# Kernel optimization log

Hardware: AMD Instinct MI355X
Metric: run time of the kernel (lower is better)

## Reference

```python
import jax, jax.numpy as jnp
import numpy as np

N = 8192
H = 256
E = N * 32
ALPHA = 0.2  # LeakyReLU negative slope from init kwarg alpha


def setup_inputs() -> dict:
    key = jax.random.key(0)
    ks = jax.random.split(key, 8)
    s = 1.0 / np.sqrt(H)
    return {
        "features": jax.random.normal(ks[0], (N, H), jnp.float32),
        "edge_index": jax.random.randint(ks[1], (2, E), 0, N, jnp.int64),
        "W_att": jax.random.normal(ks[2], (H, H), jnp.float32) * s,
        "a_src": jax.random.normal(ks[3], (H,), jnp.float32) * s,
        "a_dst": jax.random.normal(ks[4], (H,), jnp.float32) * s,
        "gcn_w": jax.random.normal(ks[5], (H, H), jnp.float32) * s,
        "gcn_b": jnp.zeros((H,), jnp.float32),
        "out_w": jax.random.normal(ks[6], (H, 2), jnp.float32) * s,
        "out_b": jnp.zeros((2,), jnp.float32),
    }


def reference(features, edge_index, W_att, a_src, a_dst, gcn_w, gcn_b, out_w, out_b):
    n = features.shape[0]
    # --- SingleNodeAttentionLayer (GAT-style dense self-attention, concat=True) ---
    Wh = features @ W_att                       # [N, H]
    e = jax.nn.leaky_relu(
        (Wh @ a_src)[:, None] + (Wh @ a_dst)[None, :], negative_slope=ALPHA
    )                                            # [N, N]
    attn = jax.nn.softmax(e, axis=-1)
    h1 = jax.nn.elu(attn @ Wh)                   # [N, H]
    # --- GCNConv: symmetric-normalized aggregation with self-loops ---
    loops = jnp.arange(n, dtype=edge_index.dtype)
    row = jnp.concatenate([edge_index[0], loops])  # destination
    col = jnp.concatenate([edge_index[1], loops])  # source
    deg = jax.ops.segment_sum(jnp.ones_like(row, dtype=h1.dtype), row, num_segments=n)
    dinv = jax.lax.rsqrt(jnp.maximum(deg, 1e-12))
    norm = dinv[row] * dinv[col]                 # [E+N]
    x = h1 @ gcn_w                               # [N, H]
    agg = jax.ops.segment_sum(x[col] * norm[:, None], row, num_segments=n) + gcn_b
    # --- head: linear -> mean over nodes -> softmax ---
    res = agg @ out_w + out_b                    # [N, 2]
    res = jnp.mean(res, axis=0, keepdims=True)   # [1, 2]
    return jax.nn.softmax(res, axis=-1)
```

## Files before the change

kernel.cpp:

```cpp
#include <hip/hip_runtime.h>
#include <hip/hip_bf16.h>

#define NN 8192
#define HH 256
#define EE (NN*32)
#define ALPHAC 0.2f
#define CHUNK 16
#define NCHUNK (NN/CHUNK)
#define CSPAD 1024

typedef __bf16 bf16x8 __attribute__((ext_vector_type(8)));
typedef float  f32x4  __attribute__((ext_vector_type(4)));

#define OFF_WH     0
#define OFF_S      (OFF_WH + NN*HH)
#define OFF_D      (OFF_S + NN)
#define OFF_SORTD  (OFF_D + NN)
#define OFF_PERM   (OFF_SORTD + NN)
#define OFF_EA     (OFF_PERM + NN)
#define OFF_E1     (OFF_EA + NN)
#define OFF_SAREL  (OFF_E1 + NN)
#define OFF_SBREL  (OFF_SAREL + NN)
#define OFF_ABPART (OFF_SBREL + NN)
#define OFF_CPAB   (OFF_ABPART + 2*NN*HH)
#define OFF_CSA    (OFF_CPAB + 2*(NCHUNK+1)*HH)
#define OFF_CSB    (OFF_CSA + CSPAD)
#define OFF_DEG    (OFF_CSB + CSPAD)
#define OFF_V      (OFF_DEG + NN)
#define OFF_DINV   (OFF_V + HH)
#define OFF_WNODE  (OFF_DINV + NN)
#define OFF_KEYS   (OFF_WNODE + NN)
#define OFF_FB16   (OFF_KEYS + 2*NN)
#define OFF_WT16   (OFF_FB16 + NN*HH/2)

__global__ __launch_bounds__(256) void k_prep(const float* __restrict__ features,
                                              const float* __restrict__ W_att,
                                              float* ws) {
    int bid = blockIdx.x, tid = threadIdx.x;
    if (bid < 1024) {
        int base = (bid*256 + tid)*8;
        float4 a = *(const float4*)(features + base);
        float4 b = *(const float4*)(features + base + 4);
        bf16x8 v;
        v[0]=(__bf16)a.x; v[1]=(__bf16)a.y; v[2]=(__bf16)a.z; v[3]=(__bf16)a.w;
        v[4]=(__bf16)b.x; v[5]=(__bf16)b.y; v[6]=(__bf16)b.z; v[7]=(__bf16)b.w;
        *(bf16x8*)((__bf16*)(ws + OFF_FB16) + base) = v;
    } else if (bid < 1056) {
        int idx0 = ((bid-1024)*256 + tid)*8;
        __bf16* WT = (__bf16*)(ws + OFF_WT16);
        #pragma unroll
        for (int q = 0; q < 8; ++q) {
            int idx = idx0 + q;
            int n = idx >> 8, k = idx & 255;
            WT[idx] = (__bf16)W_att[(size_t)k*HH + n];
        }
    } else {
        int z0 = ((bid-1056)*256 + tid)*8;
        #pragma unroll
        for (int q = 0; q < 8; ++q) {
            int i = z0 + q;
            if (i < NN + HH) ws[OFF_DEG + i] = 0.f;
        }
    }
}

__global__ __launch_bounds__(256) void k_gemm_deg(const int* __restrict__ ei, float* ws) {
    int bid = blockIdx.x, tid = threadIdx.x;
    if (bid < 512) {
        int mt = bid >> 2, nt = bid & 3;
        int wave = tid >> 6, lane = tid & 63;
        int ml = lane & 15, quad = lane >> 4;
        int row0 = mt*64 + wave*16;
        int n0 = nt*64;
        const __bf16* FB = (const __bf16*)(ws + OFF_FB16);
        const __bf16* WT = (const __bf16*)(ws + OFF_WT16);
        const __bf16* Ap = FB + (size_t)(row0 + ml)*HH + quad*8;
        const __bf16* B0 = WT + (size_t)(n0 +  0 + ml)*HH + quad*8;
        const __bf16* B1 = WT + (size_t)(n0 + 16 + ml)*HH + quad*8;
        const __bf16* B2 = WT + (size_t)(n0 + 32 + ml)*HH + quad*8;
        const __bf16* B3 = WT + (size_t)(n0 + 48 + ml)*HH + quad*8;
        f32x4 ac0 = {0.f,0.f,0.f,0.f}, ac1 = ac0, ac2 = ac0, ac3 = ac0;
        #pragma unroll
        for (int k0 = 0; k0 < HH; k0 += 32) {
            bf16x8 af = *(const bf16x8*)(Ap + k0);
            ac0 = __builtin_amdgcn_mfma_f32_16x16x32_bf16(af, *(const bf16x8*)(B0 + k0), ac0, 0, 0, 0);
            ac1 = __builtin_amdgcn_mfma_f32_16x16x32_bf16(af, *(const bf16x8*)(B1 + k0), ac1, 0, 0, 0);
            ac2 = __builtin_amdgcn_mfma_f32_16x16x32_bf16(af, *(const bf16x8*)(B2 + k0), ac2, 0, 0, 0);
            ac3 = __builtin_amdgcn_mfma_f32_16x16x32_bf16(af, *(const bf16x8*)(B3 + k0), ac3, 0, 0, 0);
        }
        float* Whp = ws + OFF_WH;
        #pragma unroll
        for (int r = 0; r < 4; ++r) {
            size_t grow = (size_t)(row0 + quad*4 + r)*HH + n0 + ml;
            Whp[grow +  0] = ac0[r];
            Whp[grow + 16] = ac1[r];
            Whp[grow + 32] = ac2[r];
            Whp[grow + 48] = ac3[r];
        }
    } else {
        int e = (bid - 512)*256 + tid;
        atomicAdd(ws + OFF_DEG + ei[e], 1.0f);
    }
}

__global__ __launch_bounds__(256) void k_sd_dinv2(const float* __restrict__ a_src,
                                                  const float* __restrict__ a_dst,
                                                  float* ws) {
    int bid = blockIdx.x, tid = threadIdx.x;
    if (bid < 2048) {
        int wave = tid >> 6, lane = tid & 63;
        int row = bid*4 + wave;
        const float* Wh = ws + OFF_WH;
        float4 wh = *(const float4*)(Wh + (size_t)row*HH + lane*4);
        float4 as = *(const float4*)(a_src + lane*4);
        float4 ad = *(const float4*)(a_dst + lane*4);
        float ss = wh.x*as.x + wh.y*as.y + wh.z*as.z + wh.w*as.w;
        float dd = wh.x*ad.x + wh.y*ad.y + wh.z*ad.z + wh.w*ad.w;
        #pragma unroll
        for (int off = 32; off; off >>= 1) {
            ss += __shfl_xor(ss, off);
            dd += __shfl_xor(dd, off);
        }
        if (lane == 0) {
            ws[OFF_S+row] = ss; ws[OFF_D+row] = dd;
            unsigned u = __float_as_uint(dd);
            unsigned mono = u ^ ((u & 0x80000000u) ? 0xFFFFFFFFu : 0x80000000u);
            ((unsigned long long*)(ws + OFF_KEYS))[row] =
                (((unsigned long long)mono) << 13) | (unsigned)row;
        }
    } else {
        int i = (bid - 2048)*256 + tid;
        float dv = rsqrtf(ws[OFF_DEG + i] + 1.0f);
        ws[OFF_DINV + i] = dv;
        ws[OFF_WNODE + i] = dv*dv;
    }
}

__global__ __launch_bounds__(256) void k_rank(float* ws) {
    __shared__ unsigned long long lk[NN];
    const unsigned long long* keys = (const unsigned long long*)(ws + OFF_KEYS);
    int tid = threadIdx.x;
    for (int m = tid; m < NN/2; m += 256)
        *(ulonglong2*)&lk[m*2] = *(const ulonglong2*)&keys[m*2];
    __syncthreads();
    int wave = tid >> 6, lane = tid & 63;
    int jb = blockIdx.x*16 + wave*4;
    unsigned long long kj0 = lk[jb+0], kj1 = lk[jb+1];
    unsigned long long kj2 = lk[jb+2], kj3 = lk[jb+3];
    int c0 = 0, c1 = 0, c2 = 0, c3 = 0;
    #pragma unroll 4
    for (int it = 0; it < 64; ++it) {
        ulonglong2 kq = *(const ulonglong2*)&lk[(it*64 + lane)*2];
        c0 += (kq.x < kj0); c1 += (kq.x < kj1);
        c2 += (kq.x < kj2); c3 += (kq.x < kj3);
        c0 += (kq.y < kj0); c1 += (kq.y < kj1);
        c2 += (kq.y < kj2); c3 += (kq.y < kj3);
    }
    #pragma unroll
    for (int off = 1; off < 64; off <<= 1) {
        c0 += __shfl_xor(c0, off);
        c1 += __shfl_xor(c1, off);
        c2 += __shfl_xor(c2, off);
        c3 += __shfl_xor(c3, off);
    }
    if (lane == 0) {
        unsigned long long kk[4] = {kj0, kj1, kj2, kj3};
        int cr[4] = {c0, c1, c2, c3};
        #pragma unroll
        for (int q = 0; q < 4; ++q) {
            unsigned long long kv = kk[q];
            int r = cr[q];
            unsigned mm = (unsigned)(kv >> 13);
            unsigned u = (mm & 0x80000000u) ? (mm ^ 0x80000000u) : ~mm;
            float dj = __uint_as_float(u);
            int j = (int)(kv & 8191ULL);
            ws[OFF_SORTD + r] = dj;
            ((int*)ws)[OFF_PERM + r] = j;
            ws[OFF_EA + r] = expf(ALPHAC * dj);
            ws[OFF_E1 + r] = expf(dj);
        }
    }
}

__global__ __launch_bounds__(256) void k_wnode_vecpref(const int* __restrict__ ei, float* ws) {
    int bid = blockIdx.x, tid = threadIdx.x;
    if (bid < NCHUNK) {
        __shared__ int   sp[CHUNK];
        __shared__ float sea[CHUNK], se1[CHUNK];
        int c = bid, h = tid;
        int k0 = c * CHUNK;
        if (h < CHUNK) {
            sp[h]  = ((int*)ws)[OFF_PERM + k0 + h];
            sea[h] = ws[OFF_EA + k0 + h];
            se1[h] = ws[OFF_E1 + k0 + h];
        }
        __syncthreads();
        if (tid < 64) {
            int lane = tid;
            float v = 0.f;
            if (lane < 16) v = sea[lane];
            else if (lane < 32) v = se1[lane-16];
            #pragma unroll
            for (int off = 1; off < 16; off <<= 1) {
                float x = __shfl_up(v, off);
                if ((lane & 15) >= off) v += x;
            }
            if (lane < 16) {
                ws[OFF_SAREL + k0 + lane] = v;
                if (lane == 15) ws[OFF_CSA + c + 1] = v;
            } else if (lane < 32) {
                ws[OFF_SBREL + k0 + lane - 16] = v;
                if (lane == 31) ws[OFF_CSB + c + 1] = v;
            }
        }
        const float* Wh = ws + OFF_WH;
        float wv[CHUNK];
        #pragma unroll
        for (int kk = 0; kk < CHUNK; ++kk)
            wv[kk] = Wh[(size_t)sp[kk]*HH + h];
        float2* abp = (float2*)(ws + OFF_ABPART);
        float acca = 0.f, accb = 0.f;
        #pragma unroll
        for (int kk = 0; kk < CHUNK; ++kk) {
            acca += sea[kk]*wv[kk]; accb += se1[kk]*wv[kk];
            abp[(size_t)(k0+kk)*HH + h] = make_float2(acca, accb);
        }
        float2* cp = (float2*)(ws + OFF_CPAB);
        cp[(size_t)(c+1)*HH + h] = make_float2(acca, accb);
    } else {
        int e = (bid - NCHUNK)*256 + tid;
        int r = ei[e], cix = ei[EE + e];
        atomicAdd(ws + OFF_WNODE + cix, ws[OFF_DINV + r] * ws[OFF_DINV + cix]);
    }
}

__global__ __launch_bounds__(256) void k_chunkscan(float* ws) {
    int bid = blockIdx.x, tid = threadIdx.x;
    if (bid < 32) {
        int h = bid*8 + (tid >> 5);
        int t = tid & 31;
        float2* cp = (float2*)(ws + OFF_CPAB);
        float la[16], lb[16];
        float ta = 0.f, tb = 0.f;
        #pragma unroll
        for (int m = 0; m < 16; ++m) {
            float2 v = cp[(size_t)(t*16 + m + 1)*HH + h];
            la[m] = v.x; lb[m] = v.y;
            ta += la[m]; tb += lb[m];
        }
        float ia = ta, ib = tb;
        #pragma unroll
        for (int off = 1; off < 32; off <<= 1) {
            float xa = __shfl_up(ia, off, 32);
            float xb = __shfl_up(ib, off, 32);
            if (t >= off) { ia += xa; ib += xb; }
        }
        float ba = ia - ta, bb = ib - tb;
        __syncthreads();
        #pragma unroll
        for (int m = 0; m < 16; ++m) {
            cp[(size_t)(t*16 + m)*HH + h] = make_float2(ba, bb);
            ba += la[m]; bb += lb[m];
        }
        if (t == 31) cp[(size_t)NCHUNK*HH + h] = make_float2(ba, bb);
    } else {
        int lane = tid & 63, wvi = tid >> 6;
        bool act = wvi < 2;
        float* cs = ws + (wvi == 1 ? OFF_CSB : OFF_CSA);
        float la[8];
        float ta = 0.f;
        if (act) {
            #pragma unroll
            for (int m = 0; m < 8; ++m) { la[m] = cs[lane*8 + m + 1]; ta += la[m]; }
        }
        float ia = ta;
        #pragma unroll
        for (int off = 1; off < 64; off <<= 1) {
            float x = __shfl_up(ia, off);
            if (lane >= off) ia += x;
        }
        float ba = ia - ta;
        __syncthreads();
        if (act) {
            #pragma unroll
            for (int m = 0; m < 8; ++m) { cs[lane*8 + m] = ba; ba += la[m]; }
            if (lane == 63) cs[NCHUNK] = ba;
        }
    }
}

__device__ __forceinline__ float elu1(float x) {
    return x > 0.f ? x : (expf(x) - 1.f);
}

__global__ __launch_bounds__(256) void k_rows(float* ws) {
    __shared__ float sd[NN];
    __shared__ float red[4][256];
    int tid = threadIdx.x;
    for (int m = tid; m < NN/4; m += 256)
        *(float4*)&sd[m*4] = *(const float4*)(ws + OFF_SORTD + m*4);
    __syncthreads();
    int wave = tid >> 6, lane = tid & 63;
    int gw = blockIdx.x*4 + wave;
    const float2* abp  = (const float2*)(ws + OFF_ABPART);
    const float2* cpab = (const float2*)(ws + OFF_CPAB);
    float btot = ws[OFF_CSB + NCHUNK];
    const float4* btr = (const float4*)(cpab + (size_t)NCHUNK*HH);
    float4 bt0 = btr[lane*2], bt1 = btr[lane*2+1];
    float BTx = bt0.y, BTy = bt0.w, BTz = bt1.y, BTw = bt1.w;

    int myr = lane & 3;
    float si_m = ws[OFF_S + gw*4 + myr];
    float tt = -si_m;
    int lo = 0, hi = NN;
    while (lo < hi) {
        int mid = (lo + hi) >> 1;
        if (sd[mid] <= tt) lo = mid + 1; else hi = mid;
    }

    float accx = 0.f, accy = 0.f, accz = 0.f, accw = 0.f;
    #pragma unroll
    for (int r = 0; r < 4; ++r) {
        int i = gw*4 + r;
        int k = __shfl(lo, r);
        float si = __shfl(si_m, r);
        float eas = expf(ALPHAC * si), es = expf(si);
        float av = 0.f, bv = 0.f;
        float Ax=0.f, Ay=0.f, Az=0.f, Aw=0.f, Bx=0.f, By=0.f, Bz=0.f, Bw=0.f;
        if (k > 0) {
            int km = k - 1, cc = km >> 4;
            av = ws[OFF_CSA + cc] + ws[OFF_SAREL + km];
            bv = ws[OFF_CSB + cc] + ws[OFF_SBREL + km];
            const float4* pr = (const float4*)(abp + (size_t)km*HH);
            const float4* cr = (const float4*)(cpab + (size_t)cc*HH);
            float4 p0 = pr[lane*2], p1 = pr[lane*2+1];
            float4 q0 = cr[lane*2], q1 = cr[lane*2+1];
            Ax = p0.x + q0.x; Bx = p0.y + q0.y;
            Ay = p0.z + q0.z; By = p0.w + q0.w;
            Az = p1.x + q1.x; Bz = p1.y + q1.y;
            Aw = p1.z + q1.z; Bw = p1.w + q1.w;
        }
        float Z = eas*av + es*(btot - bv);
        float invZ = 1.f / Z;
        float w = ws[OFF_WNODE + i];
        accx += w * elu1((eas*Ax + es*(BTx - Bx)) * invZ);
        accy += w * elu1((eas*Ay + es*(BTy - By)) * invZ);
        accz += w * elu1((eas*Az + es*(BTz - Bz)) * invZ);
        accw += w * elu1((eas*Aw + es*(BTw - Bw)) * invZ);
    }
    red[wave][lane*4+0] = accx;
    red[wave][lane*4+1] = accy;
    red[wave][lane*4+2] = accz;
    red[wave][lane*4+3] = accw;
    __syncthreads();
    float sum = red[0][tid] + red[1][tid] + red[2][tid] + red[3][tid];
    atomicAdd(ws + OFF_V + tid, sum);
}

__global__ void k_final(const float* __restrict__ gcn_w, const float* __restrict__ gcn_b,
                        const float* __restrict__ out_w, const float* __restrict__ out_b,
                        float* ws, float* out) {
    __shared__ float vl[HH];
    __shared__ float r0s[256], r1s[256];
    int t = threadIdx.x;
    vl[t] = ws[OFF_V + t];
    __syncthreads();
    float acc = 0.f;
    for (int h = 0; h < HH; ++h) acc += vl[h] * gcn_w[(size_t)h*HH + t];
    float meanv = acc * (1.0f/(float)NN) + gcn_b[t];
    r0s[t] = meanv * out_w[t*2+0];
    r1s[t] = meanv * out_w[t*2+1];
    __syncthreads();
    for (int off = 128; off; off >>= 1) {
        if (t < off) { r0s[t] += r0s[t+off]; r1s[t] += r1s[t+off]; }
        __syncthreads();
    }
    if (t == 0) {
        float res0 = r0s[0] + out_b[0], res1 = r1s[0] + out_b[1];
        float m = fmaxf(res0, res1);
        float e0 = expf(res0 - m), e1v = expf(res1 - m);
        float inv = 1.f / (e0 + e1v);
        out[0] = e0 * inv;
        out[1] = e1v * inv;
    }
}

extern "C" void kernel_launch(void* const* d_in, const int* in_sizes, int n_in,
                              void* d_out, int out_size, void* d_ws, size_t ws_size,
                              hipStream_t stream) {
    const float* features = (const float*)d_in[0];
    const int*   eidx     = (const int*)d_in[1];
    const float* W_att    = (const float*)d_in[2];
    const float* a_src    = (const float*)d_in[3];
    const float* a_dst    = (const float*)d_in[4];
    const float* gcn_w    = (const float*)d_in[5];
    const float* gcn_b    = (const float*)d_in[6];
    const float* out_w    = (const float*)d_in[7];
    const float* out_b    = (const float*)d_in[8];
    float* ws  = (float*)d_ws;
    float* out = (float*)d_out;

    k_prep<<<1061, 256, 0, stream>>>(features, W_att, ws);
    k_gemm_deg<<<1536, 256, 0, stream>>>(eidx, ws);
    k_sd_dinv2<<<2080, 256, 0, stream>>>(a_src, a_dst, ws);
    k_rank<<<NN/16, 256, 0, stream>>>(ws);
    k_wnode_vecpref<<<NCHUNK + 1024, 256, 0, stream>>>(eidx, ws);
    k_chunkscan<<<33, 256, 0, stream>>>(ws);
    k_rows<<<NN/16, 256, 0, stream>>>(ws);
    k_final<<<1, 256, 0, stream>>>(gcn_w, gcn_b, out_w, out_b, ws, out);
}
```

Baseline: 162.5 us.

## Fuse kernels, precompute W·a vectors, move threshold search into rank kernel

Computes the attention score vectors as features·(W_att·a) instead of reading Wh, which lets the score pass be fused into the GEMM/degree kernel and drops the separate score kernel. The per-row softmax split index is now counted inside the rank kernel, so the shared-memory binary search in the row kernel goes away. The final reduction becomes a last-block step in the row kernel, guarded by an atomic counter. Edge atomics now handle two edges per thread, and one redundant barrier is removed. Launches drop from eight to six, at the cost of a different fp32 summation order for the scores and a new inter-block completion protocol.

```diff
diff --git a/kernel.cpp b/kernel.cpp
--- a/kernel.cpp
+++ b/kernel.cpp
@@ -32,11 +32,28 @@
 #define OFF_KEYS   (OFF_WNODE + NN)
 #define OFF_FB16   (OFF_KEYS + 2*NN)
 #define OFF_WT16   (OFF_FB16 + NN*HH/2)
+#define OFF_CNT    (OFF_WT16 + HH*HH/2)
+#define OFF_KI     (OFF_CNT + 16)
+#define OFF_WAS    (OFF_KI + NN)
+#define OFF_WAD    (OFF_WAS + HH)
+
+__device__ __forceinline__ float elu1(float x) {
+    return x > 0.f ? x : (expf(x) - 1.f);
+}
+
+__device__ __forceinline__ unsigned long long thresh_key(float t) {
+    unsigned u = __float_as_uint(t);
+    unsigned mono = u ^ ((u & 0x80000000u) ? 0xFFFFFFFFu : 0x80000000u);
+    return ((unsigned long long)mono + 1ULL) << 13;
+}
 
 __global__ __launch_bounds__(256) void k_prep(const float* __restrict__ features,
                                               const float* __restrict__ W_att,
+                                              const float* __restrict__ a_src,
+                                              const float* __restrict__ a_dst,
                                               float* ws) {
     int bid = blockIdx.x, tid = threadIdx.x;
+    int wave = tid >> 6, lane = tid & 63;
     if (bid < 1024) {
         int base = (bid*256 + tid)*8;
         float4 a = *(const float4*)(features + base);
@@ -54,21 +71,35 @@
             int n = idx >> 8, k = idx & 255;
             WT[idx] = (__bf16)W_att[(size_t)k*HH + n];
         }
+    } else if (bid < 1120) {
+        int k = (bid - 1056)*4 + wave;
+        float4 w = *(const float4*)(W_att + (size_t)k*HH + lane*4);
+        float4 as = *(const float4*)(a_src + lane*4);
+        float4 ad = *(const float4*)(a_dst + lane*4);
+        float ss = w.x*as.x + w.y*as.y + w.z*as.z + w.w*as.w;
+        float dd = w.x*ad.x + w.y*ad.y + w.z*ad.z + w.w*ad.w;
+        #pragma unroll
+        for (int off = 32; off; off >>= 1) {
+            ss += __shfl_xor(ss, off);
+            dd += __shfl_xor(dd, off);
+        }
+        if (lane == 0) {
+            ws[OFF_WAS + k] = ss;
+            ws[OFF_WAD + k] = dd;
+        }
     } else {
-        int z0 = ((bid-1056)*256 + tid)*8;
-        #pragma unroll
-        for (int q = 0; q < 8; ++q) {
-            int i = z0 + q;
-            if (i < NN + HH) ws[OFF_DEG + i] = 0.f;
-        }
-    }
-}
-
-__global__ __launch_bounds__(256) void k_gemm_deg(const int* __restrict__ ei, float* ws) {
+        int z0 = ((bid-1120)*256 + tid);
+        if (z0 < NN + HH) ws[OFF_DEG + z0] = 0.f;
+        if (bid == 1120 && tid < 16) ((unsigned*)(ws + OFF_CNT))[tid] = 0u;
+    }
+}
+
+__global__ __launch_bounds__(256) void k_gemm_deg_sd(const float* __restrict__ features,
+                                                     const int* __restrict__ ei, float* ws) {
     int bid = blockIdx.x, tid = threadIdx.x;
+    int wave = tid >> 6, lane = tid & 63;
     if (bid < 512) {
         int mt = bid >> 2, nt = bid & 3;
-        int wave = tid >> 6, lane = tid & 63;
         int ml = lane & 15, quad = lane >> 4;
         int row0 = mt*64 + wave*16;
         int n0 = nt*64;
@@ -98,87 +129,100 @@
             Whp[grow + 48] = ac3[r];
         }
     } else {
-        int e = (bid - 512)*256 + tid;
+        int b = bid - 512;
+        int e = b*512 + tid;
         atomicAdd(ws + OFF_DEG + ei[e], 1.0f);
-    }
-}
-
-__global__ __launch_bounds__(256) void k_sd_dinv2(const float* __restrict__ a_src,
-                                                  const float* __restrict__ a_dst,
-                                                  float* ws) {
+        atomicAdd(ws + OFF_DEG + ei[e + 256], 1.0f);
+        float4 as = *(const float4*)(ws + OFF_WAS + lane*4);
+        float4 ad = *(const float4*)(ws + OFF_WAD + lane*4);
+        int row0 = b*16 + wave*4;
+        #pragma unroll
+        for (int r = 0; r < 4; ++r) {
+            int row = row0 + r;
+            float4 f = *(const float4*)(features + (size_t)row*HH + lane*4);
+            float ss = f.x*as.x + f.y*as.y + f.z*as.z + f.w*as.w;
+            float dd = f.x*ad.x + f.y*ad.y + f.z*ad.z + f.w*ad.w;
+            #pragma unroll
+            for (int off = 32; off; off >>= 1) {
+                ss += __shfl_xor(ss, off);
+                dd += __shfl_xor(dd, off);
+            }
+            if (lane == 0) {
+                ws[OFF_S+row] = ss; ws[OFF_D+row] = dd;
+                unsigned u = __float_as_uint(dd);
+                unsigned mono = u ^ ((u & 0x80000000u) ? 0xFFFFFFFFu : 0x80000000u);
+                ((unsigned long long*)(ws + OFF_KEYS))[row] =
+                    (((unsigned long long)mono) << 13) | (unsigned)row;
+            }
+        }
+    }
+}
+
+__global__ __launch_bounds__(256) void k_rank_dinv(float* ws) {
+    __shared__ unsigned long long lk[NN];
     int bid = blockIdx.x, tid = threadIdx.x;
-    if (bid < 2048) {
-        int wave = tid >> 6, lane = tid & 63;
-        int row = bid*4 + wave;
-        const float* Wh = ws + OFF_WH;
-        float4 wh = *(const float4*)(Wh + (size_t)row*HH + lane*4);
-        float4 as = *(const float4*)(a_src + lane*4);
-        float4 ad = *(const float4*)(a_dst + lane*4);
-        float ss = wh.x*as.x + wh.y*as.y + wh.z*as.z + wh.w*as.w;
-        float dd = wh.x*ad.x + wh.y*ad.y + wh.z*ad.z + wh.w*ad.w;
-        #pragma unroll
-        for (int off = 32; off; off >>= 1) {
-            ss += __shfl_xor(ss, off);
-            dd += __shfl_xor(dd, off);
+    int wave = tid >> 6, lane = tid & 63;
+    if (bid < 512) {
+        const unsigned long long* keys = (const unsigned long long*)(ws + OFF_KEYS);
+        for (int m = tid; m < NN/2; m += 256)
+            *(ulonglong2*)&lk[m*2] = *(const ulonglong2*)&keys[m*2];
+        __syncthreads();
+        int jb = bid*16 + wave*4;
+        unsigned long long kj0 = lk[jb+0], kj1 = lk[jb+1];
+        unsigned long long kj2 = lk[jb+2], kj3 = lk[jb+3];
+        unsigned long long tk0 = thresh_key(-ws[OFF_S + jb+0]);
+        unsigned long long tk1 = thresh_key(-ws[OFF_S + jb+1]);
+        unsigned long long tk2 = thresh_key(-ws[OFF_S + jb+2]);
+        unsigned long long tk3 = thresh_key(-ws[OFF_S + jb+3]);
+        int c0 = 0, c1 = 0, c2 = 0, c3 = 0;
+        int t0 = 0, t1 = 0, t2 = 0, t3 = 0;
+        #pragma unroll 4
+        for (int it = 0; it < 64; ++it) {
+            ulonglong2 kq = *(const ulonglong2*)&lk[(it*64 + lane)*2];
+            c0 += (kq.x < kj0); c1 += (kq.x < kj1);
+            c2 += (kq.x < kj2); c3 += (kq.x < kj3);
+            t0 += (kq.x < tk0); t1 += (kq.x < tk1);
+            t2 += (kq.x < tk2); t3 += (kq.x < tk3);
+            c0 += (kq.y < kj0); c1 += (kq.y < kj1);
+            c2 += (kq.y < kj2); c3 += (kq.y < kj3);
+            t0 += (kq.y < tk0); t1 += (kq.y < tk1);
+            t2 += (kq.y < tk2); t3 += (kq.y < tk3);
+        }
+        #pragma unroll
+        for (int off = 1; off < 64; off <<= 1) {
+            c0 += __shfl_xor(c0, off);
+            c1 += __shfl_xor(c1, off);
+            c2 += __shfl_xor(c2, off);
+            c3 += __shfl_xor(c3, off);
+            t0 += __shfl_xor(t0, off);
+            t1 += __shfl_xor(t1, off);
+            t2 += __shfl_xor(t2, off);
+            t3 += __shfl_xor(t3, off);
         }
         if (lane == 0) {
-            ws[OFF_S+row] = ss; ws[OFF_D+row] = dd;
-            unsigned u = __float_as_uint(dd);
-            unsigned mono = u ^ ((u & 0x80000000u) ? 0xFFFFFFFFu : 0x80000000u);
-            ((unsigned long long*)(ws + OFF_KEYS))[row] =
-                (((unsigned long long)mono) << 13) | (unsigned)row;
+            unsigned long long kk[4] = {kj0, kj1, kj2, kj3};
+            int cr[4] = {c0, c1, c2, c3};
+            int tr[4] = {t0, t1, t2, t3};
+            #pragma unroll
+            for (int q = 0; q < 4; ++q) {
+                unsigned long long kv = kk[q];
+                int r = cr[q];
+                unsigned mm = (unsigned)(kv >> 13);
+                unsigned u = (mm & 0x80000000u) ? (mm ^ 0x80000000u) : ~mm;
+                float dj = __uint_as_float(u);
+                int j = (int)(kv & 8191ULL);
+                ws[OFF_SORTD + r] = dj;
+                ((int*)ws)[OFF_PERM + r] = j;
+                ws[OFF_EA + r] = expf(ALPHAC * dj);
+                ws[OFF_E1 + r] = expf(dj);
+                ((int*)ws)[OFF_KI + jb + q] = tr[q];
+            }
         }
     } else {
-        int i = (bid - 2048)*256 + tid;
+        int i = (bid - 512)*256 + tid;
         float dv = rsqrtf(ws[OFF_DEG + i] + 1.0f);
         ws[OFF_DINV + i] = dv;
         ws[OFF_WNODE + i] = dv*dv;
-    }
-}
-
-__global__ __launch_bounds__(256) void k_rank(float* ws) {
-    __shared__ unsigned long long lk[NN];
-    const unsigned long long* keys = (const unsigned long long*)(ws + OFF_KEYS);
-    int tid = threadIdx.x;
-    for (int m = tid; m < NN/2; m += 256)
-        *(ulonglong2*)&lk[m*2] = *(const ulonglong2*)&keys[m*2];
-    __syncthreads();
-    int wave = tid >> 6, lane = tid & 63;
-    int jb = blockIdx.x*16 + wave*4;
-    unsigned long long kj0 = lk[jb+0], kj1 = lk[jb+1];
-    unsigned long long kj2 = lk[jb+2], kj3 = lk[jb+3];
-    int c0 = 0, c1 = 0, c2 = 0, c3 = 0;
-    #pragma unroll 4
-    for (int it = 0; it < 64; ++it) {
-        ulonglong2 kq = *(const ulonglong2*)&lk[(it*64 + lane)*2];
-        c0 += (kq.x < kj0); c1 += (kq.x < kj1);
-        c2 += (kq.x < kj2); c3 += (kq.x < kj3);
-        c0 += (kq.y < kj0); c1 += (kq.y < kj1);
-        c2 += (kq.y < kj2); c3 += (kq.y < kj3);
-    }
-    #pragma unroll
-    for (int off = 1; off < 64; off <<= 1) {
-        c0 += __shfl_xor(c0, off);
-        c1 += __shfl_xor(c1, off);
-        c2 += __shfl_xor(c2, off);
-        c3 += __shfl_xor(c3, off);
-    }
-    if (lane == 0) {
-        unsigned long long kk[4] = {kj0, kj1, kj2, kj3};
-        int cr[4] = {c0, c1, c2, c3};
-        #pragma unroll
-        for (int q = 0; q < 4; ++q) {
-            unsigned long long kv = kk[q];
-            int r = cr[q];
-            unsigned mm = (unsigned)(kv >> 13);
-            unsigned u = (mm & 0x80000000u) ? (mm ^ 0x80000000u) : ~mm;
-            float dj = __uint_as_float(u);
-            int j = (int)(kv & 8191ULL);
-            ws[OFF_SORTD + r] = dj;
-            ((int*)ws)[OFF_PERM + r] = j;
-            ws[OFF_EA + r] = expf(ALPHAC * dj);
-            ws[OFF_E1 + r] = expf(dj);
-        }
     }
 }
 
@@ -228,9 +272,11 @@
         float2* cp = (float2*)(ws + OFF_CPAB);
         cp[(size_t)(c+1)*HH + h] = make_float2(acca, accb);
     } else {
-        int e = (bid - NCHUNK)*256 + tid;
-        int r = ei[e], cix = ei[EE + e];
-        atomicAdd(ws + OFF_WNODE + cix, ws[OFF_DINV + r] * ws[OFF_DINV + cix]);
+        int e = (bid - NCHUNK)*512 + tid;
+        int r0 = ei[e],       c0i = ei[EE + e];
+        int r1 = ei[e + 256], c1i = ei[EE + e + 256];
+        atomicAdd(ws + OFF_WNODE + c0i, ws[OFF_DINV + r0] * ws[OFF_DINV + c0i]);
+        atomicAdd(ws + OFF_WNODE + c1i, ws[OFF_DINV + r1] * ws[OFF_DINV + c1i]);
     }
 }
 
@@ -256,7 +302,6 @@
             if (t >= off) { ia += xa; ib += xb; }
         }
         float ba = ia - ta, bb = ib - tb;
-        __syncthreads();
         #pragma unroll
         for (int m = 0; m < 16; ++m) {
             cp[(size_t)(t*16 + m)*HH + h] = make_float2(ba, bb);
@@ -289,17 +334,14 @@
     }
 }
 
-__device__ __forceinline__ float elu1(float x) {
-    return x > 0.f ? x : (expf(x) - 1.f);
-}
-
-__global__ __launch_bounds__(256) void k_rows(float* ws) {
-    __shared__ float sd[NN];
+__global__ __launch_bounds__(256) void k_rows_final(
+        const float* __restrict__ gcn_w, const float* __restrict__ gcn_b,
+        const float* __restrict__ out_w, const float* __restrict__ out_b,
+        float* ws, float* out) {
     __shared__ float red[4][256];
+    __shared__ float fin[3*256];
+    __shared__ int islast;
     int tid = threadIdx.x;
-    for (int m = tid; m < NN/4; m += 256)
-        *(float4*)&sd[m*4] = *(const float4*)(ws + OFF_SORTD + m*4);
-    __syncthreads();
     int wave = tid >> 6, lane = tid & 63;
     int gw = blockIdx.x*4 + wave;
     const float2* abp  = (const float2*)(ws + OFF_ABPART);
@@ -309,21 +351,12 @@
     float4 bt0 = btr[lane*2], bt1 = btr[lane*2+1];
     float BTx = bt0.y, BTy = bt0.w, BTz = bt1.y, BTw = bt1.w;
 
-    int myr = lane & 3;
-    float si_m = ws[OFF_S + gw*4 + myr];
-    float tt = -si_m;
-    int lo = 0, hi = NN;
-    while (lo < hi) {
-        int mid = (lo + hi) >> 1;
-        if (sd[mid] <= tt) lo = mid + 1; else hi = mid;
-    }
-
     float accx = 0.f, accy = 0.f, accz = 0.f, accw = 0.f;
     #pragma unroll
     for (int r = 0; r < 4; ++r) {
         int i = gw*4 + r;
-        int k = __shfl(lo, r);
-        float si = __shfl(si_m, r);
+        int k = ((const int*)ws)[OFF_KI + i];
+        float si = ws[OFF_S + i];
         float eas = expf(ALPHAC * si), es = expf(si);
         float av = 0.f, bv = 0.f;
         float Ax=0.f, Ay=0.f, Az=0.f, Aw=0.f, Bx=0.f, By=0.f, Bz=0.f, Bw=0.f;
@@ -355,33 +388,41 @@
     __syncthreads();
     float sum = red[0][tid] + red[1][tid] + red[2][tid] + red[3][tid];
     atomicAdd(ws + OFF_V + tid, sum);
-}
-
-__global__ void k_final(const float* __restrict__ gcn_w, const float* __restrict__ gcn_b,
-                        const float* __restrict__ out_w, const float* __restrict__ out_b,
-                        float* ws, float* out) {
-    __shared__ float vl[HH];
-    __shared__ float r0s[256], r1s[256];
-    int t = threadIdx.x;
-    vl[t] = ws[OFF_V + t];
+
     __syncthreads();
-    float acc = 0.f;
-    for (int h = 0; h < HH; ++h) acc += vl[h] * gcn_w[(size_t)h*HH + t];
-    float meanv = acc * (1.0f/(float)NN) + gcn_b[t];
-    r0s[t] = meanv * out_w[t*2+0];
-    r1s[t] = meanv * out_w[t*2+1];
+    if (tid == 0) {
+        unsigned* cnt = (unsigned*)(ws + OFF_CNT);
+        unsigned arrived = __hip_atomic_fetch_add(&cnt[0], 1u,
+                               __ATOMIC_ACQ_REL, __HIP_MEMORY_SCOPE_AGENT) + 1u;
+        islast = (arrived == (unsigned)(NN/16));
+    }
     __syncthreads();
-    for (int off = 128; off; off >>= 1) {
-        if (t < off) { r0s[t] += r0s[t+off]; r1s[t] += r1s[t+off]; }
+    if (islast) {
+        float* vl  = fin;
+        float* r0s = fin + 256;
+        float* r1s = fin + 512;
+        int t = tid;
+        vl[t] = __hip_atomic_load(ws + OFF_V + t, __ATOMIC_RELAXED,
+                                  __HIP_MEMORY_SCOPE_AGENT);
         __syncthreads();
-    }
-    if (t == 0) {
-        float res0 = r0s[0] + out_b[0], res1 = r1s[0] + out_b[1];
-        float m = fmaxf(res0, res1);
-        float e0 = expf(res0 - m), e1v = expf(res1 - m);
-        float inv = 1.f / (e0 + e1v);
-        out[0] = e0 * inv;
-        out[1] = e1v * inv;
+        float acc = 0.f;
+        for (int h = 0; h < HH; ++h) acc += vl[h] * gcn_w[(size_t)h*HH + t];
+        float meanv = acc * (1.0f/(float)NN) + gcn_b[t];
+        r0s[t] = meanv * out_w[t*2+0];
+        r1s[t] = meanv * out_w[t*2+1];
+        __syncthreads();
+        for (int off = 128; off; off >>= 1) {
+            if (t < off) { r0s[t] += r0s[t+off]; r1s[t] += r1s[t+off]; }
+            __syncthreads();
+        }
+        if (t == 0) {
+            float res0 = r0s[0] + out_b[0], res1 = r1s[0] + out_b[1];
+            float m = fmaxf(res0, res1);
+            float e0 = expf(res0 - m), e1v = expf(res1 - m);
+            float inv = 1.f / (e0 + e1v);
+            out[0] = e0 * inv;
+            out[1] = e1v * inv;
+        }
     }
 }
 
@@ -400,12 +441,10 @@
     float* ws  = (float*)d_ws;
     float* out = (float*)d_out;
 
-    k_prep<<<1061, 256, 0, stream>>>(features, W_att, ws);
-    k_gemm_deg<<<1536, 256, 0, stream>>>(eidx, ws);
-    k_sd_dinv2<<<2080, 256, 0, stream>>>(a_src, a_dst, ws);
-    k_rank<<<NN/16, 256, 0, stream>>>(ws);
-    k_wnode_vecpref<<<NCHUNK + 1024, 256, 0, stream>>>(eidx, ws);
+    k_prep<<<1154, 256, 0, stream>>>(features, W_att, a_src, a_dst, ws);
+    k_gemm_deg_sd<<<1024, 256, 0, stream>>>(features, eidx, ws);
+    k_rank_dinv<<<544, 256, 0, stream>>>(ws);
+    k_wnode_vecpref<<<1024, 256, 0, stream>>>(eidx, ws);
     k_chunkscan<<<33, 256, 0, stream>>>(ws);
-    k_rows<<<NN/16, 256, 0, stream>>>(ws);
-    k_final<<<1, 256, 0, stream>>>(gcn_w, gcn_b, out_w, out_b, ws, out);
-}
+    k_rows_final<<<NN/16, 256, 0, stream>>>(gcn_w, gcn_b, out_w, out_b, ws, out);
+}
```

New measurement: 165.3 us. Within noise of the previous version (+1.7%).
